# Optimization experiments

Hardware: AMD Instinct MI355X
Metric: run time of the kernel (lower is better)

The kernel has to match this reference:

```python
import jax, jax.numpy as jnp
import numpy as np

B, C, HH, WW, HEADS = 4, 64, 256, 256, 8
CH = C // HEADS              # 8 per-head dim
HID = int(C * 2.66)          # 170
EPS_LN = 1e-5
EPS = 1e-6
QK_NORM = 1.0
# crpe windows for 8 heads: {3:2, 5:3, 7:3}; each conv input split = head_split*Ch*2
WINDOWS = [(3, 2), (5, 3), (7, 3)]


def conv2d(x, w, b=None, groups=1, pad=0):
    out = jax.lax.conv_general_dilated(
        x, w, (1, 1), [(pad, pad), (pad, pad)],
        dimension_numbers=('NCHW', 'OIHW', 'NCHW'), feature_group_count=groups)
    return out if b is None else out + b[None, :, None, None]


def setup_inputs() -> dict:
    key = jax.random.key(0)
    ks = jax.random.split(key, 32)
    p = lambda k, shp, s=0.05: jax.random.normal(k, shp, jnp.float32) * s
    inp = {
        'x': jax.random.normal(ks[0], (B, HH * WW, C), jnp.float32),
        'ln1_w': jnp.ones((C,), jnp.float32) + p(ks[1], (C,), 0.01),
        'sca_w': p(ks[2], (C, C, 1, 1)), 'sca_b': p(ks[3], (C,)),
        'dw1_w': p(ks[4], (2 * C, C, 1, 1)),          # 1x1 dim->2dim
        'dw2_w': p(ks[5], (C, 2, 3, 3)),              # grouped 3x3, groups=C, in/grp=2
        'qkv_w': p(ks[6], (3 * C, C, 1, 1)),
        'qkv_dw_w': p(ks[7], (3 * C, 1, 3, 3)),       # depthwise 3x3
        'temperature': jnp.ones((HEADS, 1, 1), jnp.float32),
        'r3_w': p(ks[8], (2, 2 * CH, 3, 3)), 'r3_b': p(ks[9], (2,)),
        'r5_w': p(ks[10], (3, 2 * CH, 5, 5)), 'r5_b': p(ks[11], (3,)),
        'r7_w': p(ks[12], (3, 2 * CH, 7, 7)), 'r7_b': p(ks[13], (3,)),
        'proj_w': p(ks[14], (C, C, 1, 1)),
        'ln2_w': jnp.ones((C,), jnp.float32) + p(ks[15], (C,), 0.01),
        'pin_w': p(ks[16], (2 * HID, C, 1, 1)),
        'ffn_dw_w': p(ks[17], (2 * HID, 1, 3, 3)),
        'pout_w': p(ks[18], (C, HID, 1, 1)),
        'H': HH, 'W': WW,
    }
    return inp


def biasfree_ln(x, w):
    # BiasFree LayerNorm over channel dim of NCHW (var only, no mean-subtract)
    sigma = jnp.var(x, axis=1, keepdims=True)
    return x / jnp.sqrt(sigma + EPS_LN) * w[None, :, None, None]


def refine_att(q, k, H, W, convs):
    # q: (B,h,N,Ch)  k: (B,h,Ch,N) -> per-head conv relative position map (B,h,N,1)
    b, h, N, Ch = q.shape
    q_img = q.transpose(0, 1, 3, 2).reshape(b, h, Ch, H, W)
    k_img = k.reshape(b, h, Ch, H, W)
    qk = jnp.concatenate([q_img, k_img], axis=2).reshape(b, h * 2 * Ch, H, W)
    splits = np.cumsum([s * 2 * Ch for _, s in WINDOWS])[:-1]
    parts = jnp.split(qk, splits, axis=1)
    outs = [conv2d(xp, wt, bs, groups=g, pad=win // 2)
            for (win, g), (wt, bs), xp in zip(WINDOWS, convs, parts)]
    att = jnp.concatenate(outs, axis=1)           # (b, h, H, W)
    return att.reshape(b, h, 1, H * W).transpose(0, 1, 3, 2)  # (b,h,N,1)


def attention(x, sca_w, sca_b, dw1_w, dw2_w, qkv_w, qkv_dw_w, temperature,
              refine_convs, proj_w, H, W):
    b, c, _, _ = x.shape
    N = H * W
    xsca = conv2d(jnp.mean(x, axis=(2, 3), keepdims=True), sca_w, sca_b)
    x1 = conv2d(conv2d(x, dw1_w), dw2_w, groups=c, pad=1)
    qkv = conv2d(conv2d(x, qkv_w), qkv_dw_w, groups=3 * c, pad=1)
    q, k, v = jnp.split(qkv, 3, axis=1)
    q = q.reshape(b, HEADS, CH, N).transpose(0, 1, 3, 2)  # b h N Ch
    k = k.reshape(b, HEADS, CH, N)                        # b h Ch N
    v = v.reshape(b, HEADS, CH, N).transpose(0, 1, 3, 2)  # b h N Ch
    q = q / (jnp.linalg.norm(q, axis=-1, keepdims=True) / QK_NORM + EPS)
    k = k / (jnp.linalg.norm(k, axis=-2, keepdims=True) / QK_NORM + EPS)
    refine_w = jax.nn.sigmoid(refine_att(q, k, H, W, refine_convs))
    attn = k @ v                                           # b h Ch Ch
    out_num = jnp.sum(v, axis=-2, keepdims=True) + q @ attn
    ksum = jnp.sum(k, axis=-1, keepdims=True)              # b h Ch 1
    out_den = jnp.asarray(N, q.dtype) + q @ ksum + EPS     # b h N 1 (bcast to Ch)
    out = out_num / out_den * temperature
    out = out * refine_w
    out = out.transpose(0, 1, 3, 2).reshape(b, c, H, W)
    out = out * xsca * jax.nn.gelu(x1, approximate=False)
    return conv2d(out, proj_w)


def feedforward(x, pin_w, ffn_dw_w, pout_w):
    h = conv2d(x, pin_w)
    h = conv2d(h, ffn_dw_w, groups=2 * HID, pad=1)
    h1, h2 = jnp.split(h, 2, axis=1)
    return conv2d(jax.nn.gelu(h1, approximate=False) * h2, pout_w)


def reference(x, ln1_w, sca_w, sca_b, dw1_w, dw2_w, qkv_w, qkv_dw_w, temperature,
              r3_w, r3_b, r5_w, r5_b, r7_w, r7_b, proj_w, ln2_w,
              pin_w, ffn_dw_w, pout_w, H, W):
    b = x.shape[0]
    xi = x.reshape(b, H, W, C).transpose(0, 3, 1, 2)  # NCHW
    refine_convs = [(r3_w, r3_b), (r5_w, r5_b), (r7_w, r7_b)]
    xi = xi + attention(biasfree_ln(xi, ln1_w), sca_w, sca_b, dw1_w, dw2_w,
                        qkv_w, qkv_dw_w, temperature, refine_convs, proj_w, H, W)
    xi = xi + feedforward(biasfree_ln(xi, ln2_w), pin_w, ffn_dw_w, pout_w)
    return xi
```

## Files before the change

kernel.cpp:

```cpp
#include <hip/hip_runtime.h>
#include <math.h>
#include <stdio.h>

#define BB 4
#define NP 65536

typedef unsigned short u16;
typedef unsigned int u32;
typedef __attribute__((ext_vector_type(8))) short short8;
typedef __attribute__((ext_vector_type(4))) float f32x4;
typedef __attribute__((ext_vector_type(2))) float f32x2;

__device__ __forceinline__ float bf2f(u16 u) { return __uint_as_float((u32)u << 16); }
__device__ __forceinline__ u16 f2bf(float f) {
  u32 u = __float_as_uint(f);
  u = (u + 0x7FFFu + ((u >> 16) & 1u)) >> 16;
  return (u16)u;
}
__device__ __forceinline__ float gelu_f(float x) {
  return 0.5f * x * (1.f + erff(x * 0.70710678118654752f));
}

__global__ __launch_bounds__(256) void k_trans_stats(const float* __restrict__ x,
                                                     float* __restrict__ xi,
                                                     u16* __restrict__ xb1,
                                                     float* __restrict__ meanraw) {
  __shared__ float tile[64 * 65];
  __shared__ float s1a[64], s2a[64], sig[64], cm[64];
  int b = blockIdx.y;
  long n0 = (long)blockIdx.x * 64;
  int t = threadIdx.x;
  for (int i = t; i < 4096; i += 256) {
    int nl = i >> 6, c = i & 63;
    tile[nl * 65 + c] = x[((long)b * NP + n0 + nl) * 64 + c];
  }
  if (t < 64) { s1a[t] = 0.f; s2a[t] = 0.f; cm[t] = 0.f; }
  __syncthreads();
  {
    int nl = t & 63, part = t >> 6;
    float p1 = 0.f, p2 = 0.f;
    for (int cc = 0; cc < 16; cc++) {
      float v = tile[nl * 65 + part * 16 + cc];
      p1 += v; p2 += v * v;
    }
    atomicAdd(&s1a[nl], p1); atomicAdd(&s2a[nl], p2);
  }
  __syncthreads();
  if (t < 64) {
    float m = s1a[t] * (1.f / 64.f);
    float var = s2a[t] * (1.f / 64.f) - m * m;
    sig[t] = rsqrtf(var + 1e-5f);
  }
  __syncthreads();
  int nl = t & 63;
  int part = t >> 6;
  float sgv = sig[nl];
  for (int j = 0; j < 16; j++) {
    int i = t + 256 * j;
    int c = i >> 6;
    float v = tile[nl * 65 + c];
    xi[((long)b * 64 + c) * NP + n0 + nl] = v;
    float a = v * sgv;
    for (int off = 32; off; off >>= 1) a += __shfl_down(a, off);
    if ((t & 63) == 0) atomicAdd(&cm[c], a);
  }
  {
    u16* rp = xb1 + ((long)b * NP + n0 + nl) * 64 + part * 16;
    uint4 pk[2];
    u32 tmp[8];
#pragma unroll
    for (int g = 0; g < 2; g++) {
#pragma unroll
      for (int e = 0; e < 4; e++) {
        float v0 = tile[nl * 65 + part * 16 + g * 8 + 2 * e] * sgv;
        float v1 = tile[nl * 65 + part * 16 + g * 8 + 2 * e + 1] * sgv;
        tmp[e] = (u32)f2bf(v0) | ((u32)f2bf(v1) << 16);
      }
      pk[g].x = tmp[0]; pk[g].y = tmp[1]; pk[g].z = tmp[2]; pk[g].w = tmp[3];
      *(uint4*)(rp + g * 8) = pk[g];
    }
  }
  __syncthreads();
  if (t < 64) atomicAdd(&meanraw[b * 64 + t], cm[t]);
}

__global__ void k_xsca(const float* __restrict__ meanraw, const float* __restrict__ lnw,
                       const float* __restrict__ sca_w, const float* __restrict__ sca_b,
                       float* __restrict__ xsca) {
  int t = threadIdx.x;
  int b = t >> 6, co = t & 63;
  float a = sca_b[co];
  for (int ci = 0; ci < 64; ci++)
    a += sca_w[co * 64 + ci] * meanraw[b * 64 + ci] * lnw[ci] * (1.f / 65536.f);
  xsca[t] = a;
}

__global__ void k_foldW1b(const float* __restrict__ qkv_w, const float* __restrict__ dw1_w,
                          const float* __restrict__ lnw, u16* __restrict__ W1b) {
  int i = blockIdx.x * 256 + threadIdx.x;
  if (i < 320 * 64) {
    int co = i >> 6, ci = i & 63;
    float w = (co < 192) ? qkv_w[co * 64 + ci] : dw1_w[(co - 192) * 64 + ci];
    W1b[i] = f2bf(w * lnw[ci]);
  }
}
__global__ void k_foldW2b(const float* __restrict__ pin_w, const float* __restrict__ lnw,
                          u16* __restrict__ W2b) {
  int i = blockIdx.x * 256 + threadIdx.x;
  if (i < 384 * 64) {
    int co = i >> 6, ci = i & 63;
    float v = 0.f;
    if (co < 340) {
      int pair = co >> 1, which = co & 1;
      v = pin_w[(pair + which * 170) * 64 + ci] * lnw[ci];
    }
    W2b[i] = f2bf(v);
  }
}
__global__ void k_foldWpb(const float* __restrict__ w, u16* __restrict__ Wpb) {
  int i = blockIdx.x * 256 + threadIdx.x;
  if (i < 4096) Wpb[i] = f2bf(w[i]);
}
__global__ void k_tpoutb(const float* __restrict__ w, u16* __restrict__ Wob) {
  int i = blockIdx.x * 256 + threadIdx.x;
  if (i < 64 * 192) {
    int co = i / 192, ci = i - co * 192;
    Wob[i] = (ci < 170) ? f2bf(w[co * 170 + ci]) : (u16)0;
  }
}

template <int EPI>
__global__ __launch_bounds__(256) void k_mgemm(const u16* __restrict__ in, long in_bs,
                                               const u16* __restrict__ W,
                                               u16* __restrict__ outp, long out_bs,
                                               float* __restrict__ xo,
                                               u16* __restrict__ xb2r) {
  int t = threadIdx.x;
  int lane = t & 63, wv = t >> 6;
  int l15 = lane & 15, quad = lane >> 4;
  int pxw = blockIdx.x * 256 + wv * 64;
  int co0 = blockIdx.y * 64;
  int b = blockIdx.z;
  const u16* inb = in + (long)b * in_bs;

  short8 aw[4][2];
#pragma unroll
  for (int t4 = 0; t4 < 4; t4++)
#pragma unroll
    for (int kf = 0; kf < 2; kf++)
      aw[t4][kf] = *(const short8*)(W + (long)(co0 + t4 * 16 + l15) * 64 + kf * 32 + quad * 8);

  f32x4 acc[4][4];
#pragma unroll
  for (int t4 = 0; t4 < 4; t4++)
#pragma unroll
    for (int p = 0; p < 4; p++) acc[t4][p] = (f32x4){0.f, 0.f, 0.f, 0.f};

#pragma unroll
  for (int p = 0; p < 4; p++) {
    long px = pxw + p * 16 + l15;
    short8 bf0 = *(const short8*)(inb + px * 64 + quad * 8);
    short8 bf1 = *(const short8*)(inb + px * 64 + 32 + quad * 8);
#pragma unroll
    for (int t4 = 0; t4 < 4; t4++) {
      acc[t4][p] = __builtin_amdgcn_mfma_f32_16x16x32_bf16(aw[t4][0], bf0, acc[t4][p], 0, 0, 0);
      acc[t4][p] = __builtin_amdgcn_mfma_f32_16x16x32_bf16(aw[t4][1], bf1, acc[t4][p], 0, 0, 0);
    }
  }

  if (EPI == 0) {
    u16* ob = outp + (long)b * out_bs;
#pragma unroll
    for (int t4 = 0; t4 < 4; t4++)
#pragma unroll
      for (int p = 0; p < 4; p++) {
#pragma unroll
        for (int reg = 0; reg < 4; reg++) {
          int co = co0 + t4 * 16 + quad * 4 + reg;
          ob[(long)co * NP + pxw + p * 16 + l15] = f2bf(acc[t4][p][reg]);
        }
      }
  } else {
#pragma unroll
    for (int p = 0; p < 4; p++) {
      long px = pxw + p * 16 + l15;
      float xv[16];
      float s1 = 0.f, s2 = 0.f;
#pragma unroll
      for (int t4 = 0; t4 < 4; t4++)
#pragma unroll
        for (int reg = 0; reg < 4; reg++) {
          int co = t4 * 16 + quad * 4 + reg;
          float v = xo[((long)b * 64 + co) * NP + px] + acc[t4][p][reg];
          xv[t4 * 4 + reg] = v;
          s1 += v; s2 += v * v;
        }
      s1 += __shfl_xor(s1, 16); s2 += __shfl_xor(s2, 16);
      s1 += __shfl_xor(s1, 32); s2 += __shfl_xor(s2, 32);
      float m = s1 * (1.f / 64.f);
      float var = s2 * (1.f / 64.f) - m * m;
      float sg = rsqrtf(var + 1e-5f);
#pragma unroll
      for (int t4 = 0; t4 < 4; t4++)
#pragma unroll
        for (int reg = 0; reg < 4; reg++) {
          int co = t4 * 16 + quad * 4 + reg;
          xo[((long)b * 64 + co) * NP + px] = xv[t4 * 4 + reg];
        }
      u16* rp = xb2r + ((long)b * NP + px) * 64;
#pragma unroll
      for (int t4 = 0; t4 < 4; t4++) {
        u32 u0 = (u32)f2bf(xv[t4 * 4 + 0] * sg) | ((u32)f2bf(xv[t4 * 4 + 1] * sg) << 16);
        u32 u1 = (u32)f2bf(xv[t4 * 4 + 2] * sg) | ((u32)f2bf(xv[t4 * 4 + 3] * sg) << 16);
        uint2 pk; pk.x = u0; pk.y = u1;
        *(uint2*)(rp + t4 * 16 + quad * 4) = pk;
      }
    }
  }
}

__device__ __forceinline__ void dw4(const u16* __restrict__ img, int y, int x0, int lane,
                                    const float* __restrict__ w9, float d[4]) {
  d[0] = 0.f; d[1] = 0.f; d[2] = 0.f; d[3] = 0.f;
#pragma unroll
  for (int dy = -1; dy <= 1; dy++) {
    int r = y + dy;
    float v1, v2, v3, v4;
    if ((unsigned)r < 256u) {
      ushort4 u = *(const ushort4*)(img + r * 256 + x0);
      v1 = bf2f(u.x); v2 = bf2f(u.y); v3 = bf2f(u.z); v4 = bf2f(u.w);
    } else { v1 = 0.f; v2 = 0.f; v3 = 0.f; v4 = 0.f; }
    float v0 = __shfl_up(v4, 1);  if (lane == 0)  v0 = 0.f;
    float v5 = __shfl_down(v1, 1); if (lane == 63) v5 = 0.f;
    float w0 = w9[(dy + 1) * 3], w1 = w9[(dy + 1) * 3 + 1], w2 = w9[(dy + 1) * 3 + 2];
    d[0] += w0 * v0 + w1 * v1 + w2 * v2;
    d[1] += w0 * v1 + w1 * v2 + w2 * v3;
    d[2] += w0 * v2 + w1 * v3 + w2 * v4;
    d[3] += w0 * v3 + w1 * v4 + w2 * v5;
  }
}

__global__ __launch_bounds__(256) void k_dwqkv(const u16* __restrict__ P,
                                               const float* __restrict__ dww,
                                               u16* __restrict__ Qn, u16* __restrict__ Kn,
                                               u16* __restrict__ Vn) {
  int t = threadIdx.x;
  int lane = t & 63, wv = t >> 6;
  int by = blockIdx.y;
  int ph = by >> 3, h = by & 7;
  int b = blockIdx.z;
  int y = blockIdx.x * 4 + wv;
  int x0 = lane * 4;
  long n = (long)y * 256 + x0;
  int cbase = ph * 64 + h * 8;
  const u16* Pb = P + ((long)b * 192 + cbase) * NP;
  const float* wb = dww + cbase * 9;

  float v[8][4];
#pragma unroll
  for (int c = 0; c < 8; c++)
    dw4(Pb + (long)c * NP, y, x0, lane, wb + c * 9, v[c]);

  if (ph < 2) {
    float s2[4] = {0.f, 0.f, 0.f, 0.f};
#pragma unroll
    for (int c = 0; c < 8; c++)
#pragma unroll
      for (int j = 0; j < 4; j++) s2[j] += v[c][j] * v[c][j];
#pragma unroll
    for (int j = 0; j < 4; j++) s2[j] = 1.f / (sqrtf(s2[j]) + 1e-6f);
#pragma unroll
    for (int c = 0; c < 8; c++)
#pragma unroll
      for (int j = 0; j < 4; j++) v[c][j] *= s2[j];
  }
  u16* dst = (ph == 0) ? Qn : (ph == 1) ? Kn : Vn;
#pragma unroll
  for (int c = 0; c < 8; c++) {
    ushort4 st;
    st.x = f2bf(v[c][0]); st.y = f2bf(v[c][1]);
    st.z = f2bf(v[c][2]); st.w = f2bf(v[c][3]);
    *(ushort4*)(dst + ((long)b * 64 + h * 8 + c) * NP + n) = st;
  }
}

__global__ __launch_bounds__(256) void k_stats(const u16* __restrict__ Kn,
                                               const u16* __restrict__ Vn,
                                               float* __restrict__ stats) {
  int t = threadIdx.x;
  int lane = t & 63;
  int h = blockIdx.y, b = blockIdx.z;
  long px = (long)blockIdx.x * 1024 + t * 4;
  const u16* Kb = Kn + ((long)b * 64 + h * 8) * NP + px;
  const u16* Vb = Vn + ((long)b * 64 + h * 8) * NP + px;
  float kf[8][4], vf[8][4];
#pragma unroll
  for (int c = 0; c < 8; c++) {
    ushort4 ku = *(const ushort4*)(Kb + (long)c * NP);
    kf[c][0] = bf2f(ku.x); kf[c][1] = bf2f(ku.y);
    kf[c][2] = bf2f(ku.z); kf[c][3] = bf2f(ku.w);
  }
#pragma unroll
  for (int c = 0; c < 8; c++) {
    ushort4 vu = *(const ushort4*)(Vb + (long)c * NP);
    vf[c][0] = bf2f(vu.x); vf[c][1] = bf2f(vu.y);
    vf[c][2] = bf2f(vu.z); vf[c][3] = bf2f(vu.w);
  }
  __shared__ float sred[80];
  if (t < 80) sred[t] = 0.f;
  __syncthreads();
#pragma unroll
  for (int i = 0; i < 8; i++) {
#pragma unroll
    for (int j = 0; j < 8; j++) {
      float a = kf[i][0] * vf[j][0] + kf[i][1] * vf[j][1] +
                kf[i][2] * vf[j][2] + kf[i][3] * vf[j][3];
      a += __shfl_xor(a, 1); a += __shfl_xor(a, 2); a += __shfl_xor(a, 4);
      a += __shfl_xor(a, 8); a += __shfl_xor(a, 16); a += __shfl_xor(a, 32);
      if (lane == ((i * 8 + j) & 63)) atomicAdd(&sred[i * 8 + j], a);
    }
    {
      float a = kf[i][0] + kf[i][1] + kf[i][2] + kf[i][3];
      a += __shfl_xor(a, 1); a += __shfl_xor(a, 2); a += __shfl_xor(a, 4);
      a += __shfl_xor(a, 8); a += __shfl_xor(a, 16); a += __shfl_xor(a, 32);
      if (lane == ((64 + i) & 63)) atomicAdd(&sred[64 + i], a);
    }
    {
      float a = vf[i][0] + vf[i][1] + vf[i][2] + vf[i][3];
      a += __shfl_xor(a, 1); a += __shfl_xor(a, 2); a += __shfl_xor(a, 4);
      a += __shfl_xor(a, 8); a += __shfl_xor(a, 16); a += __shfl_xor(a, 32);
      if (lane == ((72 + i) & 63)) atomicAdd(&sred[72 + i], a);
    }
  }
  __syncthreads();
  if (t < 80) atomicAdd(&stats[((long)b * 8 + h) * 80 + t], sred[t]);
}

__global__ __launch_bounds__(256) void k_dwg(const u16* __restrict__ P,
                                             const float* __restrict__ dw2_w,
                                             u16* __restrict__ G) {
  int t = threadIdx.x;
  int lane = t & 63, wv = t >> 6;
  int c = blockIdx.y, b = blockIdx.z;
  int y = blockIdx.x * 4 + wv;
  int x0 = lane * 4;
  long n = (long)y * 256 + x0;
  const u16* Pb = P + (long)b * 128 * NP;
  float d1[4], d2[4];
  dw4(Pb + (long)(2 * c) * NP, y, x0, lane, dw2_w + c * 18, d1);
  dw4(Pb + (long)(2 * c + 1) * NP, y, x0, lane, dw2_w + c * 18 + 9, d2);
  ushort4 st;
  st.x = f2bf(gelu_f(d1[0] + d2[0])); st.y = f2bf(gelu_f(d1[1] + d2[1]));
  st.z = f2bf(gelu_f(d1[2] + d2[2])); st.w = f2bf(gelu_f(d1[3] + d2[3]));
  *(ushort4*)(G + ((long)b * 64 + c) * NP + n) = st;
}

__global__ __launch_bounds__(256) void k_dwgate(const u16* __restrict__ P,
                                                const float* __restrict__ dww,
                                                u16* __restrict__ Hb) {
  int t = threadIdx.x;
  int lane = t & 63, wv = t >> 6;
  int c = blockIdx.y, b = blockIdx.z;
  int y = blockIdx.x * 4 + wv;
  int x0 = lane * 4;
  long n = (long)y * 256 + x0;
  const u16* Pb = P + (long)b * 384 * NP;
  float d1[4], d2[4];
  dw4(Pb + (long)(2 * c) * NP, y, x0, lane, dww + c * 9, d1);
  dw4(Pb + (long)(2 * c + 1) * NP, y, x0, lane, dww + (170 + c) * 9, d2);
  ushort4 st;
  st.x = f2bf(gelu_f(d1[0]) * d2[0]); st.y = f2bf(gelu_f(d1[1]) * d2[1]);
  st.z = f2bf(gelu_f(d1[2]) * d2[2]); st.w = f2bf(gelu_f(d1[3]) * d2[3]);
  *(ushort4*)(Hb + ((long)b * 170 + c) * NP + n) = st;
}

__device__ __forceinline__ float wlo(u32 w) { return __uint_as_float(w << 16); }
__device__ __forceinline__ float whi(u32 w) { return __uint_as_float(w & 0xFFFF0000u); }

template <int WIN>
__device__ void refine2(const u16* __restrict__ Qh, const u16* __restrict__ Kh,
                        const float* __restrict__ wp, float bias,
                        float* __restrict__ ro, int y0, int x0, int lane) {
  const int R = WIN / 2;
  f32x2 a0a = {bias, bias}, a0b = {bias, bias};
  f32x2 a1a = {0.f, 0.f}, a1b = {0.f, 0.f};
#pragma unroll
  for (int ph = 0; ph < 2; ph++) {
    const u16* src = ph ? Kh : Qh;
#pragma unroll 1
    for (int ch = 0; ch < 8; ch++) {
      const u16* img = src + (long)ch * NP;
      const float* wc = wp + (ph * 8 + ch) * WIN * WIN;
#pragma unroll
      for (int r = -R; r <= 1 + R; r++) {
        int row = y0 + r;
        uint2 q; q.x = 0u; q.y = 0u;
        if ((unsigned)row < 256u) q = *(const uint2*)(img + row * 256 + x0);
        float f[4 + 2 * R];
        f[R + 0] = wlo(q.x); f[R + 1] = whi(q.x);
        f[R + 2] = wlo(q.y); f[R + 3] = whi(q.y);
        {
          u32 qly = (u32)__shfl_up((int)q.y, 1);
          u32 qrx = (u32)__shfl_down((int)q.x, 1);
          if (lane == 0)  qly = 0u;
          if (lane == 63) qrx = 0u;
          f[R - 1] = whi(qly); f[R + 4] = wlo(qrx);
          if (R >= 2) { f[R - 2] = wlo(qly); f[R + 5] = whi(qrx); }
          if (R >= 3) {
            u32 qlx = (u32)__shfl_up((int)q.x, 1);
            u32 qry = (u32)__shfl_down((int)q.y, 1);
            if (lane == 0)  qlx = 0u;
            if (lane == 63) qry = 0u;
            f[0] = whi(qlx); f[R + 6] = wlo(qry);
          }
        }
        f32x2 fp[3 + 2 * R];
#pragma unroll
        for (int i = 0; i < 3 + 2 * R; i++) fp[i] = (f32x2){f[i], f[i + 1]};
        if (r <= R) {
          const float* w0 = wc + (r + R) * WIN;
#pragma unroll
          for (int dx = 0; dx < WIN; dx++) {
            float wv = w0[dx];
            f32x2 w2 = {wv, wv};
            a0a += w2 * fp[dx];
            a0b += w2 * fp[dx + 2];
          }
        }
        if (r >= 1 - R) {
          const float* w1 = wc + (r - 1 + R) * WIN;
#pragma unroll
          for (int dx = 0; dx < WIN; dx++) {
            float wv = w1[dx];
            f32x2 w2 = {wv, wv};
            a1a += w2 * fp[dx];
            a1b += w2 * fp[dx + 2];
          }
        }
      }
    }
  }
  float4 o0, o1;
  o0.x = 1.f / (1.f + expf(-a0a.x)); o0.y = 1.f / (1.f + expf(-a0a.y));
  o0.z = 1.f / (1.f + expf(-a0b.x)); o0.w = 1.f / (1.f + expf(-a0b.y));
  o1.x = 1.f / (1.f + expf(-(a1a.x + bias))); o1.y = 1.f / (1.f + expf(-(a1a.y + bias)));
  o1.z = 1.f / (1.f + expf(-(a1b.x + bias))); o1.w = 1.f / (1.f + expf(-(a1b.y + bias)));
  *(float4*)(ro + (long)y0 * 256 + x0) = o0;
  *(float4*)(ro + (long)(y0 + 1) * 256 + x0) = o1;
}

__global__ __launch_bounds__(256) void k_refine(
    const u16* __restrict__ Qn, const u16* __restrict__ Kn,
    const float* __restrict__ r3w, const float* __restrict__ r3b,
    const float* __restrict__ r5w, const float* __restrict__ r5b,
    const float* __restrict__ r7w, const float* __restrict__ r7b,
    float* __restrict__ refW) {
  int t = threadIdx.x, lane = t & 63, wv = t >> 6;
  int u = blockIdx.x * 4 + wv;
  int h = u & 7;
  int rest = u >> 3;
  int b = rest >> 7;
  int y0 = (rest & 127) * 2;
  int x0 = lane * 4;
  const u16* Qh = Qn + ((long)b * 64 + h * 8) * NP;
  const u16* Kh = Kn + ((long)b * 64 + h * 8) * NP;
  float* ro = refW + ((long)(b * 8 + h)) * NP;
  if (h < 2)      refine2<3>(Qh, Kh, r3w + h * 16 * 9, r3b[h], ro, y0, x0, lane);
  else if (h < 5) refine2<5>(Qh, Kh, r5w + (h - 2) * 16 * 25, r5b[h - 2], ro, y0, x0, lane);
  else            refine2<7>(Qh, Kh, r7w + (h - 5) * 16 * 49, r7b[h - 5], ro, y0, x0, lane);
}

__global__ __launch_bounds__(256) void k_attn(
    const u16* __restrict__ Qn, const float* __restrict__ stats,
    const float* __restrict__ refw, const float* __restrict__ temp,
    const float* __restrict__ xsca, const u16* __restrict__ G,
    u16* __restrict__ Orows) {
  int b = blockIdx.y;
  int t = threadIdx.x;
  __shared__ float s[640];
  __shared__ float sx[64];
  for (int i = t; i < 640; i += 256) s[i] = stats[(long)b * 640 + i];
  if (t < 64) sx[t] = xsca[b * 64 + t];
  __syncthreads();
  long n = (long)blockIdx.x * 256 + t;
  u16* rp = Orows + ((long)b * NP + n) * 64;
#pragma unroll
  for (int h = 0; h < 8; h++) {
    const float* sh = s + h * 80;
    float q[8];
#pragma unroll
    for (int i = 0; i < 8; i++) q[i] = bf2f(Qn[((long)b * 64 + h * 8 + i) * NP + n]);
    float den = 65536.f + 1e-6f;
#pragma unroll
    for (int i = 0; i < 8; i++) den += q[i] * sh[64 + i];
    float tr = temp[h] * refw[((long)b * 8 + h) * NP + n] / den;
    u32 pk[4];
#pragma unroll
    for (int j2 = 0; j2 < 4; j2++) {
      float o01[2];
#pragma unroll
      for (int e = 0; e < 2; e++) {
        int j = j2 * 2 + e;
        float num = sh[72 + j];
#pragma unroll
        for (int i = 0; i < 8; i++) num += q[i] * sh[i * 8 + j];
        int ci = h * 8 + j;
        o01[e] = num * tr * sx[ci] * bf2f(G[((long)b * 64 + ci) * NP + n]);
      }
      pk[j2] = (u32)f2bf(o01[0]) | ((u32)f2bf(o01[1]) << 16);
    }
    uint4 v; v.x = pk[0]; v.y = pk[1]; v.z = pk[2]; v.w = pk[3];
    *(uint4*)(rp + h * 8) = v;
  }
}

__global__ __launch_bounds__(256) void k_pout(const u16* __restrict__ Hb,
                                              const u16* __restrict__ Wob,
                                              float* __restrict__ xo) {
  __shared__ u16 tile[64 * 196];
  int t = threadIdx.x;
  int lane = t & 63, wv = t >> 6;
  int l15 = lane & 15, quad = lane >> 4;
  int b = blockIdx.z;
  int px0 = blockIdx.x * 64;
  const u16* ib = Hb + (long)b * 170 * NP + px0;
#pragma unroll
  for (int i = 0; i < 12; i++) {
    int task = t + i * 256;
    int q = task >> 6, px = task & 63;
    int ci0 = q * 4;
    u32 w0 = 0u, w1 = 0u;
    if (ci0 < 170)     w0 = (u32)ib[(long)ci0 * NP + px];
    if (ci0 + 1 < 170) w0 |= ((u32)ib[(long)(ci0 + 1) * NP + px]) << 16;
    if (ci0 + 2 < 170) w1 = (u32)ib[(long)(ci0 + 2) * NP + px];
    if (ci0 + 3 < 170) w1 |= ((u32)ib[(long)(ci0 + 3) * NP + px]) << 16;
    uint2 pk; pk.x = w0; pk.y = w1;
    *(uint2*)(tile + px * 196 + ci0) = pk;
  }
  __syncthreads();

  f32x4 acc[4];
#pragma unroll
  for (int t4 = 0; t4 < 4; t4++) acc[t4] = (f32x4){0.f, 0.f, 0.f, 0.f};
  const u16* tb = tile + (wv * 16 + l15) * 196;
#pragma unroll
  for (int kf = 0; kf < 6; kf++) {
    union { uint2 u2[2]; short8 s8; } cv;
    cv.u2[0] = *(const uint2*)(tb + kf * 32 + quad * 8);
    cv.u2[1] = *(const uint2*)(tb + kf * 32 + quad * 8 + 4);
    short8 bfr = cv.s8;
#pragma unroll
    for (int t4 = 0; t4 < 4; t4++) {
      short8 aw = *(const short8*)(Wob + (long)(t4 * 16 + l15) * 192 + kf * 32 + quad * 8);
      acc[t4] = __builtin_amdgcn_mfma_f32_16x16x32_bf16(aw, bfr, acc[t4], 0, 0, 0);
    }
  }
  long pxg = px0 + wv * 16 + l15;
  float* xb = xo + (long)b * 64 * NP;
#pragma unroll
  for (int t4 = 0; t4 < 4; t4++)
#pragma unroll
    for (int reg = 0; reg < 4; reg++) {
      int co = t4 * 16 + quad * 4 + reg;
      xb[(long)co * NP + pxg] += acc[t4][reg];
    }
}

extern "C" void kernel_launch(void* const* d_in, const int* in_sizes, int n_in,
                              void* d_out, int out_size, void* d_ws, size_t ws_size,
                              hipStream_t stream) {
  const float* x        = (const float*)d_in[0];
  const float* ln1_w    = (const float*)d_in[1];
  const float* sca_w    = (const float*)d_in[2];
  const float* sca_b    = (const float*)d_in[3];
  const float* dw1_w    = (const float*)d_in[4];
  const float* dw2_w    = (const float*)d_in[5];
  const float* qkv_w    = (const float*)d_in[6];
  const float* qkv_dw_w = (const float*)d_in[7];
  const float* temp     = (const float*)d_in[8];
  const float* r3w = (const float*)d_in[9],  *r3b = (const float*)d_in[10];
  const float* r5w = (const float*)d_in[11], *r5b = (const float*)d_in[12];
  const float* r7w = (const float*)d_in[13], *r7b = (const float*)d_in[14];
  const float* proj_w   = (const float*)d_in[15];
  const float* ln2_w    = (const float*)d_in[16];
  const float* pin_w    = (const float*)d_in[17];
  const float* ffn_dw_w = (const float*)d_in[18];
  const float* pout_w   = (const float*)d_in[19];
  float* out = (float*)d_out;
  char* wsb = (char*)d_ws;

  const size_t Mi = 1048576;
  u16* xb1   = (u16*)(wsb);
  u16* Qn    = (u16*)(wsb + 32 * Mi);
  u16* Kn    = (u16*)(wsb + 64 * Mi);
  u16* G     = (u16*)(wsb + 96 * Mi);
  u16* Preg  = (u16*)(wsb + 128 * Mi);
  float* refW    = (float*)(wsb + 224 * Mi);
  float* Fm      = (float*)(wsb + 232 * Mi);
  float* stats   = Fm;
  float* meanraw = Fm + 2560;
  float* xscab   = Fm + 2816;
  u16* Wob       = (u16*)(Fm + 3072);
  u16* W1b = (u16*)(Fm + 13952);
  u16* W2b = W1b + 20480;
  u16* Wpb = W2b + 24576;
  u16* xb2 = xb1;
  u16* Orows = Kn;
  u16* Hb = Qn;
  u16* Vn = G;

  const size_t needed = 232 * Mi + 13952 * 4 + (20480 + 24576 + 4096) * 2;
  if (ws_size < needed) {
    fprintf(stderr, "kernel_launch: ws_size %zu < needed %zu\n", ws_size, needed);
    return;
  }

  hipMemsetAsync(stats, 0, (2560 + 256) * 4, stream);
  k_foldW1b<<<80, 256, 0, stream>>>(qkv_w, dw1_w, ln1_w, W1b);
  k_foldW2b<<<96, 256, 0, stream>>>(pin_w, ln2_w, W2b);
  k_foldWpb<<<16, 256, 0, stream>>>(proj_w, Wpb);
  k_tpoutb<<<48, 256, 0, stream>>>(pout_w, Wob);

  k_trans_stats<<<dim3(1024, BB), 256, 0, stream>>>(x, out, xb1, meanraw);
  k_xsca<<<1, 256, 0, stream>>>(meanraw, ln1_w, sca_w, sca_b, xscab);

  k_mgemm<0><<<dim3(256, 3, BB), 256, 0, stream>>>(xb1, (long)NP * 64, W1b,
                                                   Preg, 192L * NP, nullptr, nullptr);
  k_dwqkv<<<dim3(64, 24, BB), 256, 0, stream>>>(Preg, qkv_dw_w, Qn, Kn, Vn);
  k_stats<<<dim3(64, 8, BB), 256, 0, stream>>>(Kn, Vn, stats);

  k_mgemm<0><<<dim3(256, 2, BB), 256, 0, stream>>>(xb1, (long)NP * 64, W1b + 192 * 64,
                                                   Preg, 128L * NP, nullptr, nullptr);
  k_dwg<<<dim3(64, 64, BB), 256, 0, stream>>>(Preg, dw2_w, G);

  k_refine<<<dim3(1024), 256, 0, stream>>>(Qn, Kn, r3w, r3b, r5w, r5b, r7w, r7b, refW);
  k_attn<<<dim3(256, BB), 256, 0, stream>>>(Qn, stats, refW, temp, xscab, G, Orows);

  k_mgemm<1><<<dim3(256, 1, BB), 256, 0, stream>>>(Orows, (long)NP * 64, Wpb,
                                                   nullptr, 0, out, xb2);

  for (int pass = 0; pass < 2; pass++) {
    k_mgemm<0><<<dim3(256, 6, 2), 256, 0, stream>>>(xb2 + (long)pass * 2 * NP * 64,
                                                    (long)NP * 64, W2b,
                                                    Preg, 384L * NP, nullptr, nullptr);
    k_dwgate<<<dim3(64, 170, 2), 256, 0, stream>>>(Preg, ffn_dw_w,
                                                   Hb + (long)pass * 2 * 170 * NP);
  }
  k_pout<<<dim3(1024, 1, BB), 256, 0, stream>>>(Hb, Wob, out);
}
```

Before: 844.8 us.

## Compute two output rows per thread in depthwise convs and split refine by Q/K

The 3x3 depthwise helpers now produce two output rows per lane from four loaded rows using packed f32x2 FMAs. That cuts redundant row loads and halves the grid size of the dwqkv, dwg and dwgate kernels. The refine kernel is split so the Q-part and K-part convolutions run as separate work items, doubling its parallelism. Each part writes its partial sum to its own buffer, and the attention kernel adds the two sums and applies the sigmoid. This adds one extra fp32 map write and read, and refK reuses the Preg region, which is assumed free at that point.

After: 852.8 us. About the same (+1.0%).

```diff
diff --git a/kernel.cpp b/kernel.cpp
--- a/kernel.cpp
+++ b/kernel.cpp
@@ -20,6 +20,8 @@
 __device__ __forceinline__ float gelu_f(float x) {
   return 0.5f * x * (1.f + erff(x * 0.70710678118654752f));
 }
+__device__ __forceinline__ float wlo(u32 w) { return __uint_as_float(w << 16); }
+__device__ __forceinline__ float whi(u32 w) { return __uint_as_float(w & 0xFFFF0000u); }
 
 __global__ __launch_bounds__(256) void k_trans_stats(const float* __restrict__ x,
                                                      float* __restrict__ xi,
@@ -219,24 +221,42 @@
   }
 }
 
-__device__ __forceinline__ void dw4(const u16* __restrict__ img, int y, int x0, int lane,
-                                    const float* __restrict__ w9, float d[4]) {
-  d[0] = 0.f; d[1] = 0.f; d[2] = 0.f; d[3] = 0.f;
-#pragma unroll
-  for (int dy = -1; dy <= 1; dy++) {
-    int r = y + dy;
-    float v1, v2, v3, v4;
-    if ((unsigned)r < 256u) {
-      ushort4 u = *(const ushort4*)(img + r * 256 + x0);
-      v1 = bf2f(u.x); v2 = bf2f(u.y); v3 = bf2f(u.z); v4 = bf2f(u.w);
-    } else { v1 = 0.f; v2 = 0.f; v3 = 0.f; v4 = 0.f; }
-    float v0 = __shfl_up(v4, 1);  if (lane == 0)  v0 = 0.f;
-    float v5 = __shfl_down(v1, 1); if (lane == 63) v5 = 0.f;
-    float w0 = w9[(dy + 1) * 3], w1 = w9[(dy + 1) * 3 + 1], w2 = w9[(dy + 1) * 3 + 2];
-    d[0] += w0 * v0 + w1 * v1 + w2 * v2;
-    d[1] += w0 * v1 + w1 * v2 + w2 * v3;
-    d[2] += w0 * v2 + w1 * v3 + w2 * v4;
-    d[3] += w0 * v3 + w1 * v4 + w2 * v5;
+__device__ __forceinline__ void dw4x2(const u16* __restrict__ img, int y0, int x0, int lane,
+                                      const float* __restrict__ w9,
+                                      f32x2 o0[2], f32x2 o1[2]) {
+  o0[0] = (f32x2){0.f, 0.f}; o0[1] = (f32x2){0.f, 0.f};
+  o1[0] = (f32x2){0.f, 0.f}; o1[1] = (f32x2){0.f, 0.f};
+#pragma unroll
+  for (int r = -1; r <= 2; r++) {
+    int row = y0 + r;
+    uint2 q; q.x = 0u; q.y = 0u;
+    if ((unsigned)row < 256u) q = *(const uint2*)(img + row * 256 + x0);
+    u32 qly = (u32)__shfl_up((int)q.y, 1);
+    u32 qrx = (u32)__shfl_down((int)q.x, 1);
+    if (lane == 0)  qly = 0u;
+    if (lane == 63) qrx = 0u;
+    float f[6];
+    f[0] = whi(qly); f[1] = wlo(q.x); f[2] = whi(q.x);
+    f[3] = wlo(q.y); f[4] = whi(q.y); f[5] = wlo(qrx);
+    f32x2 fp[5];
+#pragma unroll
+    for (int i = 0; i < 5; i++) fp[i] = (f32x2){f[i], f[i + 1]};
+    if (r <= 1) {
+      const float* wr = w9 + (r + 1) * 3;
+#pragma unroll
+      for (int dx = 0; dx < 3; dx++) {
+        f32x2 w2 = {wr[dx], wr[dx]};
+        o0[0] += w2 * fp[dx]; o0[1] += w2 * fp[dx + 2];
+      }
+    }
+    if (r >= 0) {
+      const float* wr = w9 + r * 3;
+#pragma unroll
+      for (int dx = 0; dx < 3; dx++) {
+        f32x2 w2 = {wr[dx], wr[dx]};
+        o1[0] += w2 * fp[dx]; o1[1] += w2 * fp[dx + 2];
+      }
+    }
   }
 }
 
@@ -249,39 +269,43 @@
   int by = blockIdx.y;
   int ph = by >> 3, h = by & 7;
   int b = blockIdx.z;
-  int y = blockIdx.x * 4 + wv;
+  int y0 = (blockIdx.x * 4 + wv) * 2;
   int x0 = lane * 4;
-  long n = (long)y * 256 + x0;
   int cbase = ph * 64 + h * 8;
   const u16* Pb = P + ((long)b * 192 + cbase) * NP;
   const float* wb = dww + cbase * 9;
 
-  float v[8][4];
+  f32x2 v[8][2][2];
 #pragma unroll
   for (int c = 0; c < 8; c++)
-    dw4(Pb + (long)c * NP, y, x0, lane, wb + c * 9, v[c]);
+    dw4x2(Pb + (long)c * NP, y0, x0, lane, wb + c * 9, v[c][0], v[c][1]);
 
   if (ph < 2) {
-    float s2[4] = {0.f, 0.f, 0.f, 0.f};
-#pragma unroll
-    for (int c = 0; c < 8; c++)
-#pragma unroll
-      for (int j = 0; j < 4; j++) s2[j] += v[c][j] * v[c][j];
-#pragma unroll
-    for (int j = 0; j < 4; j++) s2[j] = 1.f / (sqrtf(s2[j]) + 1e-6f);
-#pragma unroll
-    for (int c = 0; c < 8; c++)
-#pragma unroll
-      for (int j = 0; j < 4; j++) v[c][j] *= s2[j];
+#pragma unroll
+    for (int row = 0; row < 2; row++) {
+      f32x2 s2a = {0.f, 0.f}, s2b = {0.f, 0.f};
+#pragma unroll
+      for (int c = 0; c < 8; c++) {
+        s2a += v[c][row][0] * v[c][row][0];
+        s2b += v[c][row][1] * v[c][row][1];
+      }
+      f32x2 ia, ib;
+      ia.x = 1.f / (sqrtf(s2a.x) + 1e-6f); ia.y = 1.f / (sqrtf(s2a.y) + 1e-6f);
+      ib.x = 1.f / (sqrtf(s2b.x) + 1e-6f); ib.y = 1.f / (sqrtf(s2b.y) + 1e-6f);
+#pragma unroll
+      for (int c = 0; c < 8; c++) { v[c][row][0] *= ia; v[c][row][1] *= ib; }
+    }
   }
   u16* dst = (ph == 0) ? Qn : (ph == 1) ? Kn : Vn;
 #pragma unroll
-  for (int c = 0; c < 8; c++) {
-    ushort4 st;
-    st.x = f2bf(v[c][0]); st.y = f2bf(v[c][1]);
-    st.z = f2bf(v[c][2]); st.w = f2bf(v[c][3]);
-    *(ushort4*)(dst + ((long)b * 64 + h * 8 + c) * NP + n) = st;
-  }
+  for (int c = 0; c < 8; c++)
+#pragma unroll
+    for (int row = 0; row < 2; row++) {
+      ushort4 st;
+      st.x = f2bf(v[c][row][0].x); st.y = f2bf(v[c][row][0].y);
+      st.z = f2bf(v[c][row][1].x); st.w = f2bf(v[c][row][1].y);
+      *(ushort4*)(dst + ((long)b * 64 + h * 8 + c) * NP + (long)(y0 + row) * 256 + x0) = st;
+    }
 }
 
 __global__ __launch_bounds__(256) void k_stats(const u16* __restrict__ Kn,
@@ -342,17 +366,20 @@
   int t = threadIdx.x;
   int lane = t & 63, wv = t >> 6;
   int c = blockIdx.y, b = blockIdx.z;
-  int y = blockIdx.x * 4 + wv;
+  int y0 = (blockIdx.x * 4 + wv) * 2;
   int x0 = lane * 4;
-  long n = (long)y * 256 + x0;
   const u16* Pb = P + (long)b * 128 * NP;
-  float d1[4], d2[4];
-  dw4(Pb + (long)(2 * c) * NP, y, x0, lane, dw2_w + c * 18, d1);
-  dw4(Pb + (long)(2 * c + 1) * NP, y, x0, lane, dw2_w + c * 18 + 9, d2);
-  ushort4 st;
-  st.x = f2bf(gelu_f(d1[0] + d2[0])); st.y = f2bf(gelu_f(d1[1] + d2[1]));
-  st.z = f2bf(gelu_f(d1[2] + d2[2])); st.w = f2bf(gelu_f(d1[3] + d2[3]));
-  *(ushort4*)(G + ((long)b * 64 + c) * NP + n) = st;
+  f32x2 d1r0[2], d1r1[2], d2r0[2], d2r1[2];
+  dw4x2(Pb + (long)(2 * c) * NP, y0, x0, lane, dw2_w + c * 18, d1r0, d1r1);
+  dw4x2(Pb + (long)(2 * c + 1) * NP, y0, x0, lane, dw2_w + c * 18 + 9, d2r0, d2r1);
+  u16* gp = G + ((long)b * 64 + c) * NP + (long)y0 * 256 + x0;
+  ushort4 s0, s1;
+  s0.x = f2bf(gelu_f(d1r0[0].x + d2r0[0].x)); s0.y = f2bf(gelu_f(d1r0[0].y + d2r0[0].y));
+  s0.z = f2bf(gelu_f(d1r0[1].x + d2r0[1].x)); s0.w = f2bf(gelu_f(d1r0[1].y + d2r0[1].y));
+  s1.x = f2bf(gelu_f(d1r1[0].x + d2r1[0].x)); s1.y = f2bf(gelu_f(d1r1[0].y + d2r1[0].y));
+  s1.z = f2bf(gelu_f(d1r1[1].x + d2r1[1].x)); s1.w = f2bf(gelu_f(d1r1[1].y + d2r1[1].y));
+  *(ushort4*)(gp) = s0;
+  *(ushort4*)(gp + 256) = s1;
 }
 
 __global__ __launch_bounds__(256) void k_dwgate(const u16* __restrict__ P,
@@ -361,90 +388,81 @@
   int t = threadIdx.x;
   int lane = t & 63, wv = t >> 6;
   int c = blockIdx.y, b = blockIdx.z;
-  int y = blockIdx.x * 4 + wv;
+  int y0 = (blockIdx.x * 4 + wv) * 2;
   int x0 = lane * 4;
-  long n = (long)y * 256 + x0;
   const u16* Pb = P + (long)b * 384 * NP;
-  float d1[4], d2[4];
-  dw4(Pb + (long)(2 * c) * NP, y, x0, lane, dww + c * 9, d1);
-  dw4(Pb + (long)(2 * c + 1) * NP, y, x0, lane, dww + (170 + c) * 9, d2);
-  ushort4 st;
-  st.x = f2bf(gelu_f(d1[0]) * d2[0]); st.y = f2bf(gelu_f(d1[1]) * d2[1]);
-  st.z = f2bf(gelu_f(d1[2]) * d2[2]); st.w = f2bf(gelu_f(d1[3]) * d2[3]);
-  *(ushort4*)(Hb + ((long)b * 170 + c) * NP + n) = st;
-}
-
-__device__ __forceinline__ float wlo(u32 w) { return __uint_as_float(w << 16); }
-__device__ __forceinline__ float whi(u32 w) { return __uint_as_float(w & 0xFFFF0000u); }
+  f32x2 d1r0[2], d1r1[2], d2r0[2], d2r1[2];
+  dw4x2(Pb + (long)(2 * c) * NP, y0, x0, lane, dww + c * 9, d1r0, d1r1);
+  dw4x2(Pb + (long)(2 * c + 1) * NP, y0, x0, lane, dww + (170 + c) * 9, d2r0, d2r1);
+  u16* hp = Hb + ((long)b * 170 + c) * NP + (long)y0 * 256 + x0;
+  ushort4 s0, s1;
+  s0.x = f2bf(gelu_f(d1r0[0].x) * d2r0[0].x); s0.y = f2bf(gelu_f(d1r0[0].y) * d2r0[0].y);
+  s0.z = f2bf(gelu_f(d1r0[1].x) * d2r0[1].x); s0.w = f2bf(gelu_f(d1r0[1].y) * d2r0[1].y);
+  s1.x = f2bf(gelu_f(d1r1[0].x) * d2r1[0].x); s1.y = f2bf(gelu_f(d1r1[0].y) * d2r1[0].y);
+  s1.z = f2bf(gelu_f(d1r1[1].x) * d2r1[1].x); s1.w = f2bf(gelu_f(d1r1[1].y) * d2r1[1].y);
+  *(ushort4*)(hp) = s0;
+  *(ushort4*)(hp + 256) = s1;
+}
 
 template <int WIN>
-__device__ void refine2(const u16* __restrict__ Qh, const u16* __restrict__ Kh,
-                        const float* __restrict__ wp, float bias,
-                        float* __restrict__ ro, int y0, int x0, int lane) {
+__device__ void refine1(const u16* __restrict__ src, const float* __restrict__ wp,
+                        float bias, float* __restrict__ ro, int y0, int x0, int lane) {
   const int R = WIN / 2;
   f32x2 a0a = {bias, bias}, a0b = {bias, bias};
-  f32x2 a1a = {0.f, 0.f}, a1b = {0.f, 0.f};
-#pragma unroll
-  for (int ph = 0; ph < 2; ph++) {
-    const u16* src = ph ? Kh : Qh;
+  f32x2 a1a = {bias, bias}, a1b = {bias, bias};
 #pragma unroll 1
-    for (int ch = 0; ch < 8; ch++) {
-      const u16* img = src + (long)ch * NP;
-      const float* wc = wp + (ph * 8 + ch) * WIN * WIN;
-#pragma unroll
-      for (int r = -R; r <= 1 + R; r++) {
-        int row = y0 + r;
-        uint2 q; q.x = 0u; q.y = 0u;
-        if ((unsigned)row < 256u) q = *(const uint2*)(img + row * 256 + x0);
-        float f[4 + 2 * R];
-        f[R + 0] = wlo(q.x); f[R + 1] = whi(q.x);
-        f[R + 2] = wlo(q.y); f[R + 3] = whi(q.y);
-        {
-          u32 qly = (u32)__shfl_up((int)q.y, 1);
-          u32 qrx = (u32)__shfl_down((int)q.x, 1);
-          if (lane == 0)  qly = 0u;
-          if (lane == 63) qrx = 0u;
-          f[R - 1] = whi(qly); f[R + 4] = wlo(qrx);
-          if (R >= 2) { f[R - 2] = wlo(qly); f[R + 5] = whi(qrx); }
-          if (R >= 3) {
-            u32 qlx = (u32)__shfl_up((int)q.x, 1);
-            u32 qry = (u32)__shfl_down((int)q.y, 1);
-            if (lane == 0)  qlx = 0u;
-            if (lane == 63) qry = 0u;
-            f[0] = whi(qlx); f[R + 6] = wlo(qry);
-          }
+  for (int ch = 0; ch < 8; ch++) {
+    const u16* img = src + (long)ch * NP;
+    const float* wc = wp + ch * WIN * WIN;
+#pragma unroll
+    for (int r = -R; r <= 1 + R; r++) {
+      int row = y0 + r;
+      uint2 q; q.x = 0u; q.y = 0u;
+      if ((unsigned)row < 256u) q = *(const uint2*)(img + row * 256 + x0);
+      float f[4 + 2 * R];
+      f[R + 0] = wlo(q.x); f[R + 1] = whi(q.x);
+      f[R + 2] = wlo(q.y); f[R + 3] = whi(q.y);
+      {
+        u32 qly = (u32)__shfl_up((int)q.y, 1);
+        u32 qrx = (u32)__shfl_down((int)q.x, 1);
+        if (lane == 0)  qly = 0u;
+        if (lane == 63) qrx = 0u;
+        f[R - 1] = whi(qly); f[R + 4] = wlo(qrx);
+        if (R >= 2) { f[R - 2] = wlo(qly); f[R + 5] = whi(qrx); }
+        if (R >= 3) {
+          u32 qlx = (u32)__shfl_up((int)q.x, 1);
+          u32 qry = (u32)__shfl_down((int)q.y, 1);
+          if (lane == 0)  qlx = 0u;
+          if (lane == 63) qry = 0u;
+          f[0] = whi(qlx); f[R + 6] = wlo(qry);
         }
-        f32x2 fp[3 + 2 * R];
-#pragma unroll
-        for (int i = 0; i < 3 + 2 * R; i++) fp[i] = (f32x2){f[i], f[i + 1]};
-        if (r <= R) {
-          const float* w0 = wc + (r + R) * WIN;
-#pragma unroll
-          for (int dx = 0; dx < WIN; dx++) {
-            float wv = w0[dx];
-            f32x2 w2 = {wv, wv};
-            a0a += w2 * fp[dx];
-            a0b += w2 * fp[dx + 2];
-          }
+      }
+      f32x2 fp[3 + 2 * R];
+#pragma unroll
+      for (int i = 0; i < 3 + 2 * R; i++) fp[i] = (f32x2){f[i], f[i + 1]};
+      if (r <= R) {
+        const float* w0 = wc + (r + R) * WIN;
+#pragma unroll
+        for (int dx = 0; dx < WIN; dx++) {
+          f32x2 w2 = {w0[dx], w0[dx]};
+          a0a += w2 * fp[dx];
+          a0b += w2 * fp[dx + 2];
         }
-        if (r >= 1 - R) {
-          const float* w1 = wc + (r - 1 + R) * WIN;
-#pragma unroll
-          for (int dx = 0; dx < WIN; dx++) {
-            float wv = w1[dx];
-            f32x2 w2 = {wv, wv};
-            a1a += w2 * fp[dx];
-            a1b += w2 * fp[dx + 2];
-          }
+      }
+      if (r >= 1 - R) {
+        const float* w1 = wc + (r - 1 + R) * WIN;
+#pragma unroll
+        for (int dx = 0; dx < WIN; dx++) {
+          f32x2 w2 = {w1[dx], w1[dx]};
+          a1a += w2 * fp[dx];
+          a1b += w2 * fp[dx + 2];
         }
       }
     }
   }
   float4 o0, o1;
-  o0.x = 1.f / (1.f + expf(-a0a.x)); o0.y = 1.f / (1.f + expf(-a0a.y));
-  o0.z = 1.f / (1.f + expf(-a0b.x)); o0.w = 1.f / (1.f + expf(-a0b.y));
-  o1.x = 1.f / (1.f + expf(-(a1a.x + bias))); o1.y = 1.f / (1.f + expf(-(a1a.y + bias)));
-  o1.z = 1.f / (1.f + expf(-(a1b.x + bias))); o1.w = 1.f / (1.f + expf(-(a1b.y + bias)));
+  o0.x = a0a.x; o0.y = a0a.y; o0.z = a0b.x; o0.w = a0b.y;
+  o1.x = a1a.x; o1.y = a1a.y; o1.z = a1b.x; o1.w = a1b.y;
   *(float4*)(ro + (long)y0 * 256 + x0) = o0;
   *(float4*)(ro + (long)(y0 + 1) * 256 + x0) = o1;
 }
@@ -454,25 +472,32 @@
     const float* __restrict__ r3w, const float* __restrict__ r3b,
     const float* __restrict__ r5w, const float* __restrict__ r5b,
     const float* __restrict__ r7w, const float* __restrict__ r7b,
-    float* __restrict__ refW) {
+    float* __restrict__ refQ, float* __restrict__ refK) {
   int t = threadIdx.x, lane = t & 63, wv = t >> 6;
-  int u = blockIdx.x * 4 + wv;
-  int h = u & 7;
-  int rest = u >> 3;
-  int b = rest >> 7;
-  int y0 = (rest & 127) * 2;
+  int yy = blockIdx.y;
+  int h = ((yy >> 1) + 5) & 7;
+  int ph = yy & 1;
+  int b = blockIdx.z;
+  int y0 = (blockIdx.x * 4 + wv) * 2;
   int x0 = lane * 4;
-  const u16* Qh = Qn + ((long)b * 64 + h * 8) * NP;
-  const u16* Kh = Kn + ((long)b * 64 + h * 8) * NP;
-  float* ro = refW + ((long)(b * 8 + h)) * NP;
-  if (h < 2)      refine2<3>(Qh, Kh, r3w + h * 16 * 9, r3b[h], ro, y0, x0, lane);
-  else if (h < 5) refine2<5>(Qh, Kh, r5w + (h - 2) * 16 * 25, r5b[h - 2], ro, y0, x0, lane);
-  else            refine2<7>(Qh, Kh, r7w + (h - 5) * 16 * 49, r7b[h - 5], ro, y0, x0, lane);
+  const u16* src = (ph ? Kn : Qn) + ((long)b * 64 + h * 8) * NP;
+  float* ro = (ph ? refK : refQ) + ((long)(b * 8 + h)) * NP;
+  if (h < 2) {
+    float bias = ph ? 0.f : r3b[h];
+    refine1<3>(src, r3w + h * 16 * 9 + ph * 8 * 9, bias, ro, y0, x0, lane);
+  } else if (h < 5) {
+    float bias = ph ? 0.f : r5b[h - 2];
+    refine1<5>(src, r5w + (h - 2) * 16 * 25 + ph * 8 * 25, bias, ro, y0, x0, lane);
+  } else {
+    float bias = ph ? 0.f : r7b[h - 5];
+    refine1<7>(src, r7w + (h - 5) * 16 * 49 + ph * 8 * 49, bias, ro, y0, x0, lane);
+  }
 }
 
 __global__ __launch_bounds__(256) void k_attn(
     const u16* __restrict__ Qn, const float* __restrict__ stats,
-    const float* __restrict__ refw, const float* __restrict__ temp,
+    const float* __restrict__ refQ, const float* __restrict__ refK,
+    const float* __restrict__ temp,
     const float* __restrict__ xsca, const u16* __restrict__ G,
     u16* __restrict__ Orows) {
   int b = blockIdx.y;
@@ -493,7 +518,8 @@
     float den = 65536.f + 1e-6f;
 #pragma unroll
     for (int i = 0; i < 8; i++) den += q[i] * sh[64 + i];
-    float tr = temp[h] * refw[((long)b * 8 + h) * NP + n] / den;
+    float rsum = refQ[((long)(b * 8 + h)) * NP + n] + refK[((long)(b * 8 + h)) * NP + n];
+    float tr = temp[h] / ((1.f + expf(-rsum)) * den);
     u32 pk[4];
 #pragma unroll
     for (int j2 = 0; j2 < 4; j2++) {
@@ -595,7 +621,8 @@
   u16* Kn    = (u16*)(wsb + 64 * Mi);
   u16* G     = (u16*)(wsb + 96 * Mi);
   u16* Preg  = (u16*)(wsb + 128 * Mi);
-  float* refW    = (float*)(wsb + 224 * Mi);
+  float* refQ    = (float*)(wsb + 224 * Mi);
+  float* refK    = (float*)(wsb + 128 * Mi);
   float* Fm      = (float*)(wsb + 232 * Mi);
   float* stats   = Fm;
   float* meanraw = Fm + 2560;
@@ -626,15 +653,16 @@
 
   k_mgemm<0><<<dim3(256, 3, BB), 256, 0, stream>>>(xb1, (long)NP * 64, W1b,
                                                    Preg, 192L * NP, nullptr, nullptr);
-  k_dwqkv<<<dim3(64, 24, BB), 256, 0, stream>>>(Preg, qkv_dw_w, Qn, Kn, Vn);
+  k_dwqkv<<<dim3(32, 24, BB), 256, 0, stream>>>(Preg, qkv_dw_w, Qn, Kn, Vn);
   k_stats<<<dim3(64, 8, BB), 256, 0, stream>>>(Kn, Vn, stats);
 
   k_mgemm<0><<<dim3(256, 2, BB), 256, 0, stream>>>(xb1, (long)NP * 64, W1b + 192 * 64,
                                                    Preg, 128L * NP, nullptr, nullptr);
-  k_dwg<<<dim3(64, 64, BB), 256, 0, stream>>>(Preg, dw2_w, G);
-
-  k_refine<<<dim3(1024), 256, 0, stream>>>(Qn, Kn, r3w, r3b, r5w, r5b, r7w, r7b, refW);
-  k_attn<<<dim3(256, BB), 256, 0, stream>>>(Qn, stats, refW, temp, xscab, G, Orows);
+  k_dwg<<<dim3(32, 64, BB), 256, 0, stream>>>(Preg, dw2_w, G);
+
+  k_refine<<<dim3(32, 16, BB), 256, 0, stream>>>(Qn, Kn, r3w, r3b, r5w, r5b, r7w, r7b,
+                                                 refQ, refK);
+  k_attn<<<dim3(256, BB), 256, 0, stream>>>(Qn, stats, refQ, refK, temp, xscab, G, Orows);
 
   k_mgemm<1><<<dim3(256, 1, BB), 256, 0, stream>>>(Orows, (long)NP * 64, Wpb,
                                                    nullptr, 0, out, xb2);
@@ -643,7 +671,7 @@
     k_mgemm<0><<<dim3(256, 6, 2), 256, 0, stream>>>(xb2 + (long)pass * 2 * NP * 64,
                                                     (long)NP * 64, W2b,
                                                     Preg, 384L * NP, nullptr, nullptr);
-    k_dwgate<<<dim3(64, 170, 2), 256, 0, stream>>>(Preg, ffn_dw_w,
+    k_dwgate<<<dim3(32, 170, 2), 256, 0, stream>>>(Preg, ffn_dw_w,
                                                    Hb + (long)pass * 2 * 170 * NP);
   }
   k_pout<<<dim3(1024, 1, BB), 256, 0, stream>>>(Hb, Wob, out);
```
